# Optimization experiments

Hardware: AMD Instinct MI355X
Metric: run time of the kernel (lower is better)

The kernel has to match this reference:

```python
import jax, jax.numpy as jnp
import numpy as np

L = 512      # x_len (also per-segment memory length)
B = 4        # batch
D = 512      # d_model
H = 8        # num_head
DH = 64      # d_head
MEM = 3      # mem_num (number of cached memory segments)
TOTAL = (MEM + 1) * L
SCALE = 1.0 / (DH ** 0.5)
LN_EPS = 1e-5


def setup_inputs() -> dict:
    key = jax.random.key(0)
    ks = jax.random.split(key, 12)
    f = lambda k, s: jax.random.normal(k, s, dtype=jnp.float32)
    x = f(ks[0], (L, B, D))
    memory = f(ks[1], (MEM, L, B, D))
    pos_emb = f(ks[2], (TOTAL, B, D))
    pos_bias_u = f(ks[3], (H, DH)) * 0.02
    pos_bias_v = f(ks[4], (H, DH)) * 0.02
    # segment gate: random 0/1, but current-input segment (last) always on
    ib = (jax.random.uniform(ks[5], (L, B, MEM + 1)) < 0.7).astype(jnp.float32)
    indice_bool = ib.at[:, :, MEM].set(1.0)
    # causal mask over concatenated [memory ; x] keys: mask future input positions
    qi = jnp.arange(L)[:, None]
    kj = jnp.arange(TOTAL)[None, :]
    mask = jnp.broadcast_to((kj > (MEM * L + qi))[:, :, None], (L, TOTAL, B))
    W_q = f(ks[6], (D, H * DH)) * 0.02
    W_kv = f(ks[7], (D, 2 * H * DH)) * 0.02
    W_rel = f(ks[8], (D, H * DH)) * 0.02
    W_o = f(ks[9], (H * DH, D)) * 0.02
    ln_g = jnp.ones((D,), jnp.float32)
    ln_b = jnp.zeros((D,), jnp.float32)
    return dict(x=x, memory=memory, pos_emb=pos_emb, pos_bias_u=pos_bias_u,
                pos_bias_v=pos_bias_v, mask=mask, indice_bool=indice_bool,
                W_q=W_q, W_kv=W_kv, W_rel=W_rel, W_o=W_o, ln_g=ln_g, ln_b=ln_b)


def _rel_shift(bd):
    # bd: [i, k, j, b, n]; torch _rel_shift flattens (k,j) and does the pad/view trick
    i, k, j, b, n = bd.shape
    xf = bd.reshape(i, k * j, b, n)
    zp = jnp.zeros((i, 1, b, n), bd.dtype)
    xp = jnp.concatenate([zp, xf], axis=1)            # [i, k*j+1, b, n]
    xp = xp.reshape(k * j + 1, i, b, n)               # raw memory reinterpretation
    return xp[1:].reshape(i, k, j, b, n)


def reference(x, memory, pos_emb, pos_bias_u, pos_bias_v, mask, indice_bool,
              W_q, W_kv, W_rel, W_o, ln_g, ln_b):
    Lq, Bz, Dm = x.shape
    mem_flat = memory.reshape(MEM * Lq, Bz, Dm)
    c = jnp.concatenate([mem_flat, x], axis=0)        # [TOTAL, B, D]
    kv = c @ W_kv                                     # [TOTAL, B, 2*H*DH]
    k_, v_ = jnp.split(kv, 2, axis=-1)
    pk = k_.reshape(MEM + 1, Lq, Bz, H, DH)
    pv = v_.reshape(MEM + 1, Lq, Bz, H, DH)
    rel = (pos_emb @ W_rel).reshape(MEM + 1, Lq, Bz, H, DH)
    q = (x @ W_q).reshape(Lq, Bz, H, DH)
    qu = q + pos_bias_u
    qv = q + pos_bias_v
    # gate[i,k,1,b,1] == indice_bool[i,b,k]; equals einsum('ibnd,ibk->kibnd') pre-mul
    gate = jnp.transpose(indice_bool, (0, 2, 1))[:, :, None, :, None]
    AC = jnp.einsum('ibnd,kjbnd->ikjbn', qu, pk) * gate   # [i,k,j,b,n]
    BD = jnp.einsum('ibnd,kjbnd->ikjbn', qv, rel) * gate
    BD = _rel_shift(BD)
    score = (AC + BD) * SCALE
    score = score.reshape(Lq, TOTAL, Bz, H)
    score = jnp.where(mask[:, :, :, None], -jnp.inf, score)
    prob = jax.nn.softmax(score, axis=1)
    attn_matrix = prob.mean(axis=(2, 3))              # [i, TOTAL]
    prob5 = prob.reshape(Lq, MEM + 1, Lq, Bz, H)
    vec = jnp.einsum('ikjbn,kjbnd->ibnd', prob5, pv).reshape(Lq, Bz, H * DH)
    attn_out = vec @ W_o
    y = x + attn_out
    mu = y.mean(-1, keepdims=True)
    var = jnp.mean(jnp.square(y - mu), axis=-1, keepdims=True)
    output = (y - mu) / jnp.sqrt(var + LN_EPS) * ln_g + ln_b
    return (output, attn_matrix)
```

## Files before the change

kernel.cpp:

```cpp
#include <hip/hip_runtime.h>
#include <hip/hip_bf16.h>
#include <math.h>

typedef __bf16 bhalf8 __attribute__((ext_vector_type(8)));
typedef __bf16 bhalf4 __attribute__((ext_vector_type(4)));
typedef float  f32x4  __attribute__((ext_vector_type(4)));

#define MFMA16(a, b, c) __builtin_amdgcn_mfma_f32_16x16x32_bf16(a, b, c, 0, 0, 0)

__global__ __launch_bounds__(256) void cast_bf16(const float* __restrict__ in,
                                                 __bf16* __restrict__ out, int n4)
{
  const int i = blockIdx.x * 256 + threadIdx.x;
  if (i < n4) {
    float4 v = ((const float4*)in)[i];
    bhalf4 o;
    o[0] = (__bf16)v.x; o[1] = (__bf16)v.y; o[2] = (__bf16)v.z; o[3] = (__bf16)v.w;
    ((bhalf4*)out)[i] = o;
  }
}

__global__ __launch_bounds__(256) void transcast(const float* __restrict__ W,
                                                 __bf16* __restrict__ Wt, int K, int N)
{
  const int k = blockIdx.x * 64 + (threadIdx.x & 63);
  const int n = blockIdx.y * 4 + (threadIdx.x >> 6);
  Wt[(size_t)n * K + k] = (__bf16)W[(size_t)k * N + n];
}

template <int OUT_MODE>
__global__ __launch_bounds__(256) void gemm_bf16(
    const __bf16* __restrict__ A, const __bf16* __restrict__ Bt,
    void* __restrict__ C, int M, int N, int K,
    const float* __restrict__ pbu, const float* __restrict__ pbv,
    __bf16* __restrict__ qup, __bf16* __restrict__ qvp)
{
  __shared__ __bf16 a_lds[128][40];
  __shared__ __bf16 b_lds[128][40];
  const int m0 = blockIdx.x * 128;
  const int n0 = blockIdx.y * 128;
  const int tid = threadIdx.x;
  const int w = tid >> 6, l = tid & 63;
  const int wn = (w >> 1) * 64, wm = (w & 1) * 64;
  const int li = l & 15, lq = l >> 4;
  const int lk = lq << 3;

  f32x4 acc[4][4] = {};

  for (int k0 = 0; k0 < K; k0 += 32) {
    __syncthreads();
#pragma unroll
    for (int c = 0; c < 2; ++c) {
      const int chunk = c * 256 + tid;
      const int row = chunk >> 2, kc = (chunk & 3) << 3;
      *(bhalf8*)&a_lds[row][kc] = *(const bhalf8*)(A + (size_t)(m0 + row) * K + k0 + kc);
      *(bhalf8*)&b_lds[row][kc] = *(const bhalf8*)(Bt + (size_t)(n0 + row) * K + k0 + kc);
    }
    __syncthreads();
    bhalf8 af[4], bf_[4];
#pragma unroll
    for (int s = 0; s < 4; ++s) {
      af[s]  = *(const bhalf8*)&b_lds[wn + s * 16 + li][lk];
      bf_[s] = *(const bhalf8*)&a_lds[wm + s * 16 + li][lk];
    }
#pragma unroll
    for (int ns = 0; ns < 4; ++ns)
#pragma unroll
      for (int ms = 0; ms < 4; ++ms)
        acc[ns][ms] = MFMA16(af[ns], bf_[ms], acc[ns][ms]);
  }

  const int lr = lq << 2;
#pragma unroll
  for (int ms = 0; ms < 4; ++ms) {
    const int m = m0 + wm + ms * 16 + li;
#pragma unroll
    for (int ns = 0; ns < 4; ++ns) {
      const int n = n0 + wn + ns * 16 + lr;
      if (OUT_MODE == 1) {
        *(f32x4*)((float*)C + (size_t)m * N + n) = acc[ns][ms];
      } else if (OUT_MODE == 0) {
        bhalf4 pk;
#pragma unroll
        for (int r = 0; r < 4; ++r) pk[r] = (__bf16)acc[ns][ms][r];
        *(bhalf4*)((__bf16*)C + (size_t)m * N + n) = pk;
      } else {
        const int i = m >> 2, bb = m & 3, hd = n >> 6;
        float4 u4 = *(const float4*)(pbu + n);
        float4 v4 = *(const float4*)(pbv + n);
        const size_t off = (((size_t)bb * 8 + hd) * 512 + i) * 64 + (n & 63);
        bhalf4 pu, pv;
        pu[0] = (__bf16)((acc[ns][ms][0] + u4.x) * 0.125f);
        pu[1] = (__bf16)((acc[ns][ms][1] + u4.y) * 0.125f);
        pu[2] = (__bf16)((acc[ns][ms][2] + u4.z) * 0.125f);
        pu[3] = (__bf16)((acc[ns][ms][3] + u4.w) * 0.125f);
        pv[0] = (__bf16)((acc[ns][ms][0] + v4.x) * 0.125f);
        pv[1] = (__bf16)((acc[ns][ms][1] + v4.y) * 0.125f);
        pv[2] = (__bf16)((acc[ns][ms][2] + v4.z) * 0.125f);
        pv[3] = (__bf16)((acc[ns][ms][3] + v4.w) * 0.125f);
        *(bhalf4*)(qup + off) = pu;
        *(bhalf4*)(qvp + off) = pv;
      }
    }
  }
}

__global__ __launch_bounds__(256) void vtrans(const __bf16* __restrict__ kvb,
                                              __bf16* __restrict__ vtb)
{
  __shared__ __bf16 T2[64][72];
  const int t0 = blockIdx.x * 64;
  const int p = blockIdx.y;
  const int b = p >> 3, n = p & 7;
  const int tid = threadIdx.x;
#pragma unroll
  for (int c = 0; c < 2; ++c) {
    const int e = c * 256 + tid;
    const int tl = e >> 3, d8 = (e & 7) << 3;
    bhalf8 v8 = *(const bhalf8*)(kvb + ((size_t)(t0 + tl) * 4 + b) * 1024 + 512 + n * 64 + d8);
#pragma unroll
    for (int j = 0; j < 8; ++j) T2[d8 + j][tl] = v8[j];
  }
  __syncthreads();
#pragma unroll
  for (int c = 0; c < 2; ++c) {
    const int e = c * 256 + tid;
    const int d = e >> 3, t8 = (e & 7) << 3;
    bhalf8 v = *(const bhalf8*)&T2[d][t8];
    *(bhalf8*)(vtb + ((size_t)p * 64 + d) * 2048 + t0 + t8) = v;
  }
}

__global__ __launch_bounds__(512, 4) void attn_v3(
    const __bf16* __restrict__ qup, const __bf16* __restrict__ qvp,
    const __bf16* __restrict__ kvb, const __bf16* __restrict__ relb,
    const __bf16* __restrict__ vtb, const float* __restrict__ indice,
    __bf16* __restrict__ vecb, float* __restrict__ ml,
    __bf16* __restrict__ pb, float* __restrict__ ms)
{
  __shared__ __align__(16) __bf16 P_l[32][136];
  __shared__ __align__(16) __bf16 bdl[160][33];
  __shared__ float red0[8][33];
  __shared__ float red1[8][33];
  __shared__ float lfin[32];

  const int bid = blockIdx.x;
  const int wrk = ((bid & 7) << 6) + (bid >> 3);
  const int plane = wrk >> 4;
  const int i0 = (wrk & 15) << 5;
  const int b = plane >> 3, n = plane & 7;
  const int tid = threadIdx.x;
  const int w = tid >> 6;
  const int l = tid & 63;
  const int li = l & 15;
  const int lq = l >> 4;

  const __bf16* kbase = kvb + (size_t)b * 1024 + n * 64;
  const __bf16* rbase = relb + (size_t)b * 512 + n * 64;
  const __bf16* vbase = vtb + (size_t)plane * 131072;

  bhalf8 qu[2][2], qv[2][2];
  float g[2][4];
#pragma unroll
  for (int it = 0; it < 2; ++it) {
    const int i = i0 + it * 16 + li;
    const float* gp = indice + ((size_t)i * 4 + b) * 4;
    g[it][0] = gp[0]; g[it][1] = gp[1]; g[it][2] = gp[2]; g[it][3] = gp[3];
    const __bf16* qp = qup + ((size_t)plane * 512 + i) * 64;
    const __bf16* qq = qvp + ((size_t)plane * 512 + i) * 64;
    qu[it][0] = *(const bhalf8*)(qp + lq * 8);
    qu[it][1] = *(const bhalf8*)(qp + 32 + lq * 8);
    qv[it][0] = *(const bhalf8*)(qq + lq * 8);
    qv[it][1] = *(const bhalf8*)(qq + 32 + lq * 8);
  }

  float m0 = -1e30f, m1 = -1e30f, l0 = 0.f, l1 = 0.f;
  f32x4 oacc = {0.f, 0.f, 0.f, 0.f};
  const int dgw = w >> 1, itw = w & 1;
  const int nt = ((1536 + i0 + 31) >> 7) + 1;

  for (int tile = 0; tile < nt; ++tile) {
    const int tb = tile << 7;
    const int rb = tb + 480 - i0;

#pragma unroll
    for (int ri = 0; ri < 2; ++ri) {
      const int rs = w + ri * 8;
      if (ri == 0 || rs < 10) {
        int row = rb + rs * 16 + li;
        row = row > 2047 ? 2047 : row;
        const __bf16* rp = rbase + (size_t)row * 2048;
        bhalf8 a0 = *(const bhalf8*)(rp + lq * 8);
        bhalf8 a1 = *(const bhalf8*)(rp + 32 + lq * 8);
#pragma unroll
        for (int it = 0; it < 2; ++it) {
          f32x4 c = {0.f, 0.f, 0.f, 0.f};
          c = MFMA16(a0, qv[it][0], c);
          c = MFMA16(a1, qv[it][1], c);
#pragma unroll
          for (int r = 0; r < 4; ++r) {
            const int rowl = rs * 16 + lq * 4 + r;
            int rk = (rb + rowl) >> 9; rk = rk > 3 ? 3 : rk;
            bdl[rowl][it * 16 + li] = (__bf16)(c[r] * g[it][rk]);
          }
        }
      }
    }
    f32x4 s[2];
    {
      const __bf16* kp = kbase + (size_t)(tb + w * 16 + li) * 4096;
      bhalf8 a0 = *(const bhalf8*)(kp + lq * 8);
      bhalf8 a1 = *(const bhalf8*)(kp + 32 + lq * 8);
#pragma unroll
      for (int it = 0; it < 2; ++it) {
        f32x4 c = {0.f, 0.f, 0.f, 0.f};
        c = MFMA16(a0, qu[it][0], c);
        c = MFMA16(a1, qu[it][1], c);
        s[it] = c;
      }
    }
    __syncthreads();

    float sv[2][4];
    float tmax[2] = {-1e30f, -1e30f};
#pragma unroll
    for (int it = 0; it < 2; ++it) {
      const int i = i0 + it * 16 + li;
#pragma unroll
      for (int r = 0; r < 4; ++r) {
        const int tl = w * 16 + lq * 4 + r;
        const int t = tb + tl;
        float sc = -1e30f;
        if (t <= 1536 + i) {
          const float bdv = (float)bdl[tl + 31 - it * 16 - li][it * 16 + li];
          sc = s[it][r] * g[it][t >> 9] + bdv;
        }
        sv[it][r] = sc;
        tmax[it] = fmaxf(tmax[it], sc);
      }
    }
    tmax[0] = fmaxf(tmax[0], __shfl_xor(tmax[0], 16));
    tmax[0] = fmaxf(tmax[0], __shfl_xor(tmax[0], 32));
    tmax[1] = fmaxf(tmax[1], __shfl_xor(tmax[1], 16));
    tmax[1] = fmaxf(tmax[1], __shfl_xor(tmax[1], 32));
    if (l < 16) { red0[w][li] = tmax[0]; red0[w][16 + li] = tmax[1]; }
    __syncthreads();

    float mn[2], scl[2];
#pragma unroll
    for (int it = 0; it < 2; ++it) {
      const int ic = it * 16 + li;
      float mt = red0[0][ic];
#pragma unroll
      for (int ww = 1; ww < 8; ++ww) mt = fmaxf(mt, red0[ww][ic]);
      const float mo = it ? m1 : m0;
      mn[it] = fmaxf(mo, mt);
      scl[it] = __expf(mo - mn[it]);
    }
    if (w == 0 && l < 16) {
      float* msp = ms + ((size_t)plane * 16 + tile) * 512 + i0;
      msp[li] = mn[0];
      msp[16 + li] = mn[1];
    }
    float ps[2] = {0.f, 0.f};
#pragma unroll
    for (int it = 0; it < 2; ++it) {
      bhalf4 pk;
#pragma unroll
      for (int r = 0; r < 4; ++r) {
        const float p = __expf(sv[it][r] - mn[it]);
        ps[it] += p;
        pk[r] = (__bf16)p;
      }
      *(bhalf4*)&P_l[it * 16 + li][w * 16 + lq * 4] = pk;
    }
    ps[0] += __shfl_xor(ps[0], 16); ps[0] += __shfl_xor(ps[0], 32);
    ps[1] += __shfl_xor(ps[1], 16); ps[1] += __shfl_xor(ps[1], 32);
    if (l < 16) { red1[w][li] = ps[0]; red1[w][16 + li] = ps[1]; }
    __syncthreads();

    {
      const int iloc = tid >> 4, tq = tid & 15;
      bhalf8 pv8 = *(const bhalf8*)&P_l[iloc][tq * 8];
      *(bhalf8*)(pb + ((size_t)plane * 512 + i0 + iloc) * 2048 + tb + tq * 8) = pv8;
    }

    {
      float ls0 = 0.f, ls1 = 0.f;
#pragma unroll
      for (int ww = 0; ww < 8; ++ww) { ls0 += red1[ww][li]; ls1 += red1[ww][16 + li]; }
      l0 = l0 * scl[0] + ls0; m0 = mn[0];
      l1 = l1 * scl[1] + ls1; m1 = mn[1];
    }
    oacc *= scl[itw];
    {
      const __bf16* vp = vbase + (size_t)(dgw * 16 + li) * 2048 + tb;
#pragma unroll
      for (int kt = 0; kt < 4; ++kt) {
        bhalf8 af = *(const bhalf8*)(vp + kt * 32 + lq * 8);
        bhalf8 bf_ = *(const bhalf8*)&P_l[itw * 16 + li][kt * 32 + lq * 8];
        oacc = MFMA16(af, bf_, oacc);
      }
    }
  }

  __syncthreads();
  float* obuf = (float*)&P_l[0][0];
  if (w == 0 && l < 16) {
    lfin[li] = 1.f / l0;
    lfin[16 + li] = 1.f / l1;
    float* mp0 = ml + ((size_t)plane * 512 + i0 + li) * 2;
    mp0[0] = m0; mp0[1] = l0;
    float* mp1 = ml + ((size_t)plane * 512 + i0 + 16 + li) * 2;
    mp1[0] = m1; mp1[1] = l1;
  }
#pragma unroll
  for (int r = 0; r < 4; ++r)
    obuf[(itw * 16 + li) * 68 + dgw * 16 + lq * 4 + r] = oacc[r];
  __syncthreads();
  {
    const int iloc = tid >> 4, dq = tid & 15;
    const float rli = lfin[iloc];
    f32x4 o = *(f32x4*)&obuf[iloc * 68 + dq * 4];
    bhalf4 ov;
#pragma unroll
    for (int r = 0; r < 4; ++r) ov[r] = (__bf16)(o[r] * rli);
    *(bhalf4*)(vecb + ((size_t)(i0 + iloc) * 4 + b) * 512 + n * 64 + dq * 4) = ov;
  }
}

__global__ __launch_bounds__(256) void am_final(
    const __bf16* __restrict__ pb, const float* __restrict__ ms,
    const float* __restrict__ ml, float* __restrict__ am)
{
  const int i = blockIdx.x;
  const int tid = threadIdx.x;
  const int t0 = tid << 3;
  const int tile = t0 >> 7;
  const bool valid = tile <= ((1536 + (i | 31)) >> 7);
  f32x4 a0 = {0.f, 0.f, 0.f, 0.f}, a1 = {0.f, 0.f, 0.f, 0.f};
#pragma unroll 4
  for (int p = 0; p < 32; ++p) {
    const float2 mlv = *(const float2*)(ml + ((size_t)p * 512 + i) * 2);
    float wgt = 0.f;
    if (valid)
      wgt = __expf(ms[((size_t)p * 16 + tile) * 512 + i] - mlv.x) / mlv.y;
    bhalf8 v = *(const bhalf8*)(pb + ((size_t)p * 512 + i) * 2048 + t0);
    a0[0] += wgt * (float)v[0];
    a0[1] += wgt * (float)v[1];
    a0[2] += wgt * (float)v[2];
    a0[3] += wgt * (float)v[3];
    a1[0] += wgt * (float)v[4];
    a1[1] += wgt * (float)v[5];
    a1[2] += wgt * (float)v[6];
    a1[3] += wgt * (float)v[7];
  }
  const float sc = 1.f / 32.f;
  *(f32x4*)(am + (size_t)i * 2048 + t0)     = a0 * sc;
  *(f32x4*)(am + (size_t)i * 2048 + t0 + 4) = a1 * sc;
}

__global__ __launch_bounds__(256) void ln_f32(
    const float* __restrict__ x, const float* __restrict__ ao,
    const float* __restrict__ g, const float* __restrict__ bb,
    float* __restrict__ out)
{
  const int row = blockIdx.x;
  const int tid = threadIdx.x;
  const size_t base = (size_t)row * 512;
  const float y0 = x[base + tid] + ao[base + tid];
  const float y1 = x[base + 256 + tid] + ao[base + 256 + tid];
  float s  = y0 + y1;
  float ss = y0 * y0 + y1 * y1;
#pragma unroll
  for (int off = 32; off > 0; off >>= 1) {
    s  += __shfl_xor(s, off);
    ss += __shfl_xor(ss, off);
  }
  __shared__ float sred[4], ssred[4], stat[2];
  const int w = tid >> 6;
  if ((tid & 63) == 0) { sred[w] = s; ssred[w] = ss; }
  __syncthreads();
  if (tid == 0) {
    const float S  = sred[0] + sred[1] + sred[2] + sred[3];
    const float SS = ssred[0] + ssred[1] + ssred[2] + ssred[3];
    const float mu = S * (1.f / 512.f);
    const float var = SS * (1.f / 512.f) - mu * mu;
    stat[0] = mu;
    stat[1] = rsqrtf(var + 1e-5f);
  }
  __syncthreads();
  const float mu = stat[0], rs = stat[1];
  out[base + tid]       = (y0 - mu) * rs * g[tid] + bb[tid];
  out[base + 256 + tid] = (y1 - mu) * rs * g[256 + tid] + bb[256 + tid];
}

extern "C" void kernel_launch(void* const* d_in, const int* in_sizes, int n_in,
                              void* d_out, int out_size, void* d_ws, size_t ws_size,
                              hipStream_t stream)
{
  (void)in_sizes; (void)n_in; (void)out_size; (void)ws_size;
  const float* x      = (const float*)d_in[0];
  const float* memory = (const float*)d_in[1];
  const float* pos    = (const float*)d_in[2];
  const float* pbu    = (const float*)d_in[3];
  const float* pbv    = (const float*)d_in[4];
  const float* indice = (const float*)d_in[6];
  const float* W_q    = (const float*)d_in[7];
  const float* W_kv   = (const float*)d_in[8];
  const float* W_rel  = (const float*)d_in[9];
  const float* W_o    = (const float*)d_in[10];
  const float* ln_g   = (const float*)d_in[11];
  const float* ln_b   = (const float*)d_in[12];

  float* out = (float*)d_out;
  float* am  = out + 1048576;

  __bf16* cb    = (__bf16*)d_ws;
  __bf16* posb  = cb + 4194304;
  __bf16* kvb   = posb + 4194304;
  __bf16* relb  = kvb + 8388608;
  __bf16* qup   = relb + 4194304;
  __bf16* qvp   = qup + 1048576;
  __bf16* vecb  = qvp + 1048576;
  __bf16* wqt   = vecb + 1048576;
  __bf16* wkvt  = wqt + 262144;
  __bf16* wrelt = wkvt + 524288;
  __bf16* wot   = wrelt + 262144;
  float*  ml    = (float*)(wot + 262144);
  float*  ms    = ml + 32768;
  __bf16* pbuf  = (__bf16*)(ms + 262144);
  __bf16* xb    = cb + 3145728;
  __bf16* vtb   = cb;
  float*  aof   = (float*)posb;

  cast_bf16<<<3072, 256, 0, stream>>>(memory, cb, 786432);
  cast_bf16<<<1024, 256, 0, stream>>>(x, xb, 262144);
  cast_bf16<<<4096, 256, 0, stream>>>(pos, posb, 1048576);
  transcast<<<dim3(8, 128), 256, 0, stream>>>(W_q,   wqt,   512, 512);
  transcast<<<dim3(8, 256), 256, 0, stream>>>(W_kv,  wkvt,  512, 1024);
  transcast<<<dim3(8, 128), 256, 0, stream>>>(W_rel, wrelt, 512, 512);
  transcast<<<dim3(8, 128), 256, 0, stream>>>(W_o,   wot,   512, 512);

  gemm_bf16<2><<<dim3(16, 4), 256, 0, stream>>>(xb, wqt, (void*)qup, 2048, 512, 512,
                                                pbu, pbv, qup, qvp);
  gemm_bf16<0><<<dim3(64, 8), 256, 0, stream>>>(cb, wkvt, kvb, 8192, 1024, 512,
                                                nullptr, nullptr, nullptr, nullptr);
  gemm_bf16<0><<<dim3(64, 4), 256, 0, stream>>>(posb, wrelt, relb, 8192, 512, 512,
                                                nullptr, nullptr, nullptr, nullptr);

  vtrans<<<dim3(32, 32), 256, 0, stream>>>(kvb, vtb);

  attn_v3<<<512, 512, 0, stream>>>(qup, qvp, kvb, relb, vtb, indice, vecb, ml,
                                   pbuf, ms);

  am_final<<<512, 256, 0, stream>>>(pbuf, ms, ml, am);

  gemm_bf16<1><<<dim3(16, 4), 256, 0, stream>>>(vecb, wot, aof, 2048, 512, 512,
                                                nullptr, nullptr, nullptr, nullptr);
  ln_f32<<<2048, 256, 0, stream>>>(x, aof, ln_g, ln_b, out);
}
```

Baseline: 301.6 us.

## Split attention key range across two blocks, fuse fp32 casts into GEMM loads

The attention kernel now runs twice as many blocks, each handling half of the key tiles (first 8 tiles vs the rest), writing unnormalized fp32 partial outputs and per-row max/sum. A new merge kernel combines them flash-decoding style. The separate fp32-to-bf16 cast kernels are removed by having the GEMMs load fp32 activations directly and convert while staging into LDS, including a split pointer so memory and x are read without concatenation. The four weight transpose-casts are merged into one launch. This targets low occupancy and load imbalance in attention plus extra launches and memory traffic, at the cost of fp32 partial-output traffic and one extra merge kernel.

```diff
diff --git a/kernel.cpp b/kernel.cpp
--- a/kernel.cpp
+++ b/kernel.cpp
@@ -8,30 +8,25 @@
 
 #define MFMA16(a, b, c) __builtin_amdgcn_mfma_f32_16x16x32_bf16(a, b, c, 0, 0, 0)
 
-__global__ __launch_bounds__(256) void cast_bf16(const float* __restrict__ in,
-                                                 __bf16* __restrict__ out, int n4)
-{
-  const int i = blockIdx.x * 256 + threadIdx.x;
-  if (i < n4) {
-    float4 v = ((const float4*)in)[i];
-    bhalf4 o;
-    o[0] = (__bf16)v.x; o[1] = (__bf16)v.y; o[2] = (__bf16)v.z; o[3] = (__bf16)v.w;
-    ((bhalf4*)out)[i] = o;
-  }
-}
-
-__global__ __launch_bounds__(256) void transcast(const float* __restrict__ W,
-                                                 __bf16* __restrict__ Wt, int K, int N)
-{
-  const int k = blockIdx.x * 64 + (threadIdx.x & 63);
-  const int n = blockIdx.y * 4 + (threadIdx.x >> 6);
-  Wt[(size_t)n * K + k] = (__bf16)W[(size_t)k * N + n];
-}
-
-template <int OUT_MODE>
+__global__ __launch_bounds__(256) void transcast_all(
+    const float* __restrict__ Wq, const float* __restrict__ Wkv,
+    const float* __restrict__ Wrel, const float* __restrict__ Wo,
+    __bf16* __restrict__ Wt)
+{
+  const int k  = blockIdx.x * 64 + (threadIdx.x & 63);
+  const int ng = blockIdx.y * 4 + (threadIdx.x >> 6);
+  const float* src; int nn, Ns;
+  if (ng < 512)       { src = Wq;   nn = ng;        Ns = 512; }
+  else if (ng < 1536) { src = Wkv;  nn = ng - 512;  Ns = 1024; }
+  else if (ng < 2048) { src = Wrel; nn = ng - 1536; Ns = 512; }
+  else                { src = Wo;   nn = ng - 2048; Ns = 512; }
+  Wt[(size_t)ng * 512 + k] = (__bf16)src[(size_t)k * Ns + nn];
+}
+
+template <int OUT_MODE, int A_F32>
 __global__ __launch_bounds__(256) void gemm_bf16(
-    const __bf16* __restrict__ A, const __bf16* __restrict__ Bt,
-    void* __restrict__ C, int M, int N, int K,
+    const void* __restrict__ A0v, const void* __restrict__ A1v, int split,
+    const __bf16* __restrict__ Bt, void* __restrict__ C, int M, int N, int K,
     const float* __restrict__ pbu, const float* __restrict__ pbv,
     __bf16* __restrict__ qup, __bf16* __restrict__ qvp)
 {
@@ -45,16 +40,39 @@
   const int li = l & 15, lq = l >> 4;
   const int lk = lq << 3;
 
+  const int srow0 = tid >> 2, srow1 = (tid >> 2) + 64;
+  const int skc = (tid & 3) << 3;
+  const float* arowf[2];
+  const __bf16* arowh[2];
+  if (A_F32) {
+    const float* A0 = (const float*)A0v;
+    const float* A1 = (const float*)A1v;
+    const int r0 = m0 + srow0, r1 = m0 + srow1;
+    arowf[0] = r0 < split ? A0 + (size_t)r0 * K : A1 + (size_t)(r0 - split) * K;
+    arowf[1] = r1 < split ? A0 + (size_t)r1 * K : A1 + (size_t)(r1 - split) * K;
+  } else {
+    arowh[0] = (const __bf16*)A0v + (size_t)(m0 + srow0) * K;
+    arowh[1] = (const __bf16*)A0v + (size_t)(m0 + srow1) * K;
+  }
+
   f32x4 acc[4][4] = {};
 
   for (int k0 = 0; k0 < K; k0 += 32) {
     __syncthreads();
 #pragma unroll
     for (int c = 0; c < 2; ++c) {
-      const int chunk = c * 256 + tid;
-      const int row = chunk >> 2, kc = (chunk & 3) << 3;
-      *(bhalf8*)&a_lds[row][kc] = *(const bhalf8*)(A + (size_t)(m0 + row) * K + k0 + kc);
-      *(bhalf8*)&b_lds[row][kc] = *(const bhalf8*)(Bt + (size_t)(n0 + row) * K + k0 + kc);
+      const int row = c ? srow1 : srow0;
+      if (A_F32) {
+        float4 f0 = *(const float4*)(arowf[c] + k0 + skc);
+        float4 f1 = *(const float4*)(arowf[c] + k0 + skc + 4);
+        bhalf8 h;
+        h[0] = (__bf16)f0.x; h[1] = (__bf16)f0.y; h[2] = (__bf16)f0.z; h[3] = (__bf16)f0.w;
+        h[4] = (__bf16)f1.x; h[5] = (__bf16)f1.y; h[6] = (__bf16)f1.z; h[7] = (__bf16)f1.w;
+        *(bhalf8*)&a_lds[row][skc] = h;
+      } else {
+        *(bhalf8*)&a_lds[row][skc] = *(const bhalf8*)(arowh[c] + k0 + skc);
+      }
+      *(bhalf8*)&b_lds[row][skc] = *(const bhalf8*)(Bt + (size_t)(n0 + row) * K + k0 + skc);
     }
     __syncthreads();
     bhalf8 af[4], bf_[4];
@@ -131,23 +149,23 @@
   }
 }
 
-__global__ __launch_bounds__(512, 4) void attn_v3(
+__global__ __launch_bounds__(512, 4) void attn_v4(
     const __bf16* __restrict__ qup, const __bf16* __restrict__ qvp,
     const __bf16* __restrict__ kvb, const __bf16* __restrict__ relb,
     const __bf16* __restrict__ vtb, const float* __restrict__ indice,
-    __bf16* __restrict__ vecb, float* __restrict__ ml,
+    float* __restrict__ po, float* __restrict__ mlh,
     __bf16* __restrict__ pb, float* __restrict__ ms)
 {
   __shared__ __align__(16) __bf16 P_l[32][136];
-  __shared__ __align__(16) __bf16 bdl[160][33];
+  __shared__ __align__(16) __bf16 bdl[160][34];
   __shared__ float red0[8][33];
   __shared__ float red1[8][33];
-  __shared__ float lfin[32];
 
   const int bid = blockIdx.x;
-  const int wrk = ((bid & 7) << 6) + (bid >> 3);
-  const int plane = wrk >> 4;
-  const int i0 = (wrk & 15) << 5;
+  const int wrk = ((bid & 7) << 7) | (bid >> 3);
+  const int plane = wrk >> 5;
+  const int i0 = ((wrk >> 1) & 15) << 5;
+  const int half = wrk & 1;
   const int b = plane >> 3, n = plane & 7;
   const int tid = threadIdx.x;
   const int w = tid >> 6;
@@ -178,8 +196,10 @@
   f32x4 oacc = {0.f, 0.f, 0.f, 0.f};
   const int dgw = w >> 1, itw = w & 1;
   const int nt = ((1536 + i0 + 31) >> 7) + 1;
-
-  for (int tile = 0; tile < nt; ++tile) {
+  const int t_start = half ? 8 : 0;
+  const int t_end   = half ? nt : 8;
+
+  for (int tile = t_start; tile < t_end; ++tile) {
     const int tb = tile << 7;
     const int rb = tb + 480 - i0;
 
@@ -307,11 +327,9 @@
   __syncthreads();
   float* obuf = (float*)&P_l[0][0];
   if (w == 0 && l < 16) {
-    lfin[li] = 1.f / l0;
-    lfin[16 + li] = 1.f / l1;
-    float* mp0 = ml + ((size_t)plane * 512 + i0 + li) * 2;
+    float* mp0 = mlh + ((size_t)half * 16384 + plane * 512 + i0 + li) * 2;
     mp0[0] = m0; mp0[1] = l0;
-    float* mp1 = ml + ((size_t)plane * 512 + i0 + 16 + li) * 2;
+    float* mp1 = mlh + ((size_t)half * 16384 + plane * 512 + i0 + 16 + li) * 2;
     mp1[0] = m1; mp1[1] = l1;
   }
 #pragma unroll
@@ -320,13 +338,31 @@
   __syncthreads();
   {
     const int iloc = tid >> 4, dq = tid & 15;
-    const float rli = lfin[iloc];
     f32x4 o = *(f32x4*)&obuf[iloc * 68 + dq * 4];
-    bhalf4 ov;
-#pragma unroll
-    for (int r = 0; r < 4; ++r) ov[r] = (__bf16)(o[r] * rli);
-    *(bhalf4*)(vecb + ((size_t)(i0 + iloc) * 4 + b) * 512 + n * 64 + dq * 4) = ov;
-  }
+    *(f32x4*)(po + ((size_t)half * 16384 + plane * 512 + i0 + iloc) * 64 + dq * 4) = o;
+  }
+}
+
+__global__ __launch_bounds__(256) void attn_merge(
+    const float* __restrict__ po, const float* __restrict__ mlh,
+    __bf16* __restrict__ vecb, float* __restrict__ ml)
+{
+  const int row = blockIdx.x * 16 + (threadIdx.x >> 4);
+  const int dq = threadIdx.x & 15;
+  const float2 a = *(const float2*)(mlh + (size_t)row * 2);
+  const float2 bm = *(const float2*)(mlh + ((size_t)16384 + row) * 2);
+  const float mf = fmaxf(a.x, bm.x);
+  const float ea = __expf(a.x - mf), eb = __expf(bm.x - mf);
+  const float lf = a.y * ea + bm.y * eb;
+  f32x4 oa = *(const f32x4*)(po + (size_t)row * 64 + dq * 4);
+  f32x4 ob = *(const f32x4*)(po + ((size_t)16384 + row) * 64 + dq * 4);
+  const float inv = 1.f / lf;
+  bhalf4 ov;
+#pragma unroll
+  for (int r = 0; r < 4; ++r) ov[r] = (__bf16)((oa[r] * ea + ob[r] * eb) * inv);
+  const int plane = row >> 9, i = row & 511, b = plane >> 3, n = plane & 7;
+  *(bhalf4*)(vecb + ((size_t)i * 4 + b) * 512 + n * 64 + dq * 4) = ov;
+  if (dq == 0) { ml[(size_t)row * 2] = mf; ml[(size_t)row * 2 + 1] = lf; }
 }
 
 __global__ __launch_bounds__(256) void am_final(
@@ -416,47 +452,46 @@
   float* out = (float*)d_out;
   float* am  = out + 1048576;
 
-  __bf16* cb    = (__bf16*)d_ws;
-  __bf16* posb  = cb + 4194304;
-  __bf16* kvb   = posb + 4194304;
-  __bf16* relb  = kvb + 8388608;
-  __bf16* qup   = relb + 4194304;
-  __bf16* qvp   = qup + 1048576;
-  __bf16* vecb  = qvp + 1048576;
-  __bf16* wqt   = vecb + 1048576;
-  __bf16* wkvt  = wqt + 262144;
-  __bf16* wrelt = wkvt + 524288;
-  __bf16* wot   = wrelt + 262144;
-  float*  ml    = (float*)(wot + 262144);
-  float*  ms    = ml + 32768;
-  __bf16* pbuf  = (__bf16*)(ms + 262144);
-  __bf16* xb    = cb + 3145728;
-  __bf16* vtb   = cb;
-  float*  aof   = (float*)posb;
-
-  cast_bf16<<<3072, 256, 0, stream>>>(memory, cb, 786432);
-  cast_bf16<<<1024, 256, 0, stream>>>(x, xb, 262144);
-  cast_bf16<<<4096, 256, 0, stream>>>(pos, posb, 1048576);
-  transcast<<<dim3(8, 128), 256, 0, stream>>>(W_q,   wqt,   512, 512);
-  transcast<<<dim3(8, 256), 256, 0, stream>>>(W_kv,  wkvt,  512, 1024);
-  transcast<<<dim3(8, 128), 256, 0, stream>>>(W_rel, wrelt, 512, 512);
-  transcast<<<dim3(8, 128), 256, 0, stream>>>(W_o,   wot,   512, 512);
-
-  gemm_bf16<2><<<dim3(16, 4), 256, 0, stream>>>(xb, wqt, (void*)qup, 2048, 512, 512,
-                                                pbu, pbv, qup, qvp);
-  gemm_bf16<0><<<dim3(64, 8), 256, 0, stream>>>(cb, wkvt, kvb, 8192, 1024, 512,
-                                                nullptr, nullptr, nullptr, nullptr);
-  gemm_bf16<0><<<dim3(64, 4), 256, 0, stream>>>(posb, wrelt, relb, 8192, 512, 512,
-                                                nullptr, nullptr, nullptr, nullptr);
+  __bf16* ws    = (__bf16*)d_ws;
+  __bf16* vtb   = ws;
+  float*  po    = (float*)(ws + 4194304);
+  float*  aof   = po;
+  __bf16* kvb   = ws + 8388608;
+  __bf16* relb  = ws + 16777216;
+  __bf16* qup   = ws + 20971520;
+  __bf16* qvp   = ws + 22020096;
+  __bf16* vecb  = ws + 23068672;
+  __bf16* wt    = ws + 24117248;
+  __bf16* wqt   = wt;
+  __bf16* wkvt  = wt + 512 * 512;
+  __bf16* wrelt = wt + 1536 * 512;
+  __bf16* wot   = wt + 2048 * 512;
+  float*  ml    = (float*)(ws + 25427968);
+  float*  ms    = (float*)(ws + 25493504);
+  __bf16* pbuf  = ws + 26017792;
+  float*  mlh   = (float*)(ws + 59572224);
+
+  transcast_all<<<dim3(8, 640), 256, 0, stream>>>(W_q, W_kv, W_rel, W_o, wt);
+
+  gemm_bf16<2, 1><<<dim3(16, 4), 256, 0, stream>>>(x, x, 2048, wqt, (void*)qup,
+                                                   2048, 512, 512, pbu, pbv, qup, qvp);
+  gemm_bf16<0, 1><<<dim3(64, 8), 256, 0, stream>>>(memory, x, 6144, wkvt, kvb,
+                                                   8192, 1024, 512,
+                                                   nullptr, nullptr, nullptr, nullptr);
+  gemm_bf16<0, 1><<<dim3(64, 4), 256, 0, stream>>>(pos, pos, 8192, wrelt, relb,
+                                                   8192, 512, 512,
+                                                   nullptr, nullptr, nullptr, nullptr);
 
   vtrans<<<dim3(32, 32), 256, 0, stream>>>(kvb, vtb);
 
-  attn_v3<<<512, 512, 0, stream>>>(qup, qvp, kvb, relb, vtb, indice, vecb, ml,
-                                   pbuf, ms);
+  attn_v4<<<1024, 512, 0, stream>>>(qup, qvp, kvb, relb, vtb, indice,
+                                    po, mlh, pbuf, ms);
+  attn_merge<<<1024, 256, 0, stream>>>(po, mlh, vecb, ml);
 
   am_final<<<512, 256, 0, stream>>>(pbuf, ms, ml, am);
 
-  gemm_bf16<1><<<dim3(16, 4), 256, 0, stream>>>(vecb, wot, aof, 2048, 512, 512,
-                                                nullptr, nullptr, nullptr, nullptr);
+  gemm_bf16<1, 0><<<dim3(16, 4), 256, 0, stream>>>(vecb, vecb, 2048, wot, aof,
+                                                   2048, 512, 512,
+                                                   nullptr, nullptr, nullptr, nullptr);
   ln_f32<<<2048, 256, 0, stream>>>(x, aof, ln_g, ln_b, out);
 }
```

Measured after the change: 305.1 us. About the same (+1.2%).
